# Performance work log

Hardware: AMD Instinct MI355X
Metric: run time of the kernel (lower is better)

The kernel has to match this reference:

```python
import jax, jax.numpy as jnp
import numpy as np


def _unfold(x, k):
    # x: [B, C, H, W] -> [B, C, S, L] with S=k*k (row-major patch order), L=H*W
    B, C, H, W = x.shape
    pad = k // 2
    xp = jnp.pad(x, ((0, 0), (0, 0), (pad, pad), (pad, pad)))
    patches = jnp.stack(
        [xp[:, :, r:r + H, c:c + W] for r in range(k) for c in range(k)], axis=2
    )  # [B, C, S, H, W]
    return patches.reshape(B, C, k * k, H * W)


def setup_inputs() -> dict:
    key = jax.random.key(0)
    ks = jax.random.split(key, 8)
    B, C, H, W = 8, 64, 128, 128
    R, Cout = 4, 128
    x = jax.random.normal(ks[0], (B, C, H, W), dtype=jnp.float32)
    gate_w = jax.random.normal(ks[1], (R, C), dtype=jnp.float32) * 0.05   # 1x1 gate conv weight
    gate_b = jax.random.normal(ks[2], (R,), dtype=jnp.float32) * 0.01
    theta = jax.random.normal(ks[3], (R,), dtype=jnp.float32) * 0.5       # learned directions
    raw_sigma_u = jax.random.normal(ks[4], (R,), dtype=jnp.float32) * 0.1
    raw_sigma_s = jax.random.normal(ks[5], (R,), dtype=jnp.float32) * 0.1
    pw_w = jax.random.normal(ks[6], (Cout, R * C), dtype=jnp.float32) * (1.0 / np.sqrt(R * C).astype(np.float32))
    pw_b = jax.random.normal(ks[7], (Cout,), dtype=jnp.float32) * 0.01
    return {"x": x, "gate_w": gate_w, "gate_b": gate_b, "theta": theta,
            "raw_sigma_u": raw_sigma_u, "raw_sigma_s": raw_sigma_s,
            "pw_w": pw_w, "pw_b": pw_b}


def reference(x, gate_w, gate_b, theta, raw_sigma_u, raw_sigma_s, pw_w, pw_b):
    k = 3
    B, C, H, W = x.shape
    R = theta.shape[0]
    S, L = k * k, H * W

    x_un = _unfold(x, k)                                         # [B, C, S, L]

    # 1x1 gate conv + fuzzy softmax over rules
    logits = jnp.einsum('bchw,rc->brhw', x, gate_w) + gate_b[None, :, None, None]
    mu = jax.nn.softmax(logits, axis=1)                          # [B, R, H, W]
    mu_un = _unfold(mu, k)                                       # [B, R, S, L]
    s_center = (k // 2) * k + (k // 2)
    mu_center = mu_un[:, :, s_center:s_center + 1, :]            # [B, R, 1, L]

    # anisotropic Gaussian kernel per rule over integer offsets (row-major)
    grid = np.arange(k, dtype=np.float32) - k // 2
    dy = jnp.asarray(np.repeat(grid, k))                         # [S]
    dx = jnp.asarray(np.tile(grid, k))                           # [S]
    cos_t, sin_t = jnp.cos(theta)[:, None], jnp.sin(theta)[:, None]
    proj_u = cos_t * dx[None, :] + sin_t * dy[None, :]           # [R, S]
    proj_s = -sin_t * dx[None, :] + cos_t * dy[None, :]
    su = (jax.nn.softplus(raw_sigma_u) + 1e-4)[:, None]
    ss = (jax.nn.softplus(raw_sigma_s) + 1e-4)[:, None]
    kern = jnp.exp(-proj_u ** 2 / su ** 2 - proj_s ** 2 / ss ** 2)  # [R, S]

    alpha = mu_center * mu_un * kern[None, :, :, None]           # [B, R, S, L]
    alpha_sum = jnp.maximum(alpha.sum(axis=(1, 2), keepdims=True), 1e-8)
    alpha = alpha / alpha_sum

    agg = jnp.einsum('brsl,bcsl->brcl', alpha, x_un)             # [B, R, C, L]
    agg_flat = agg.reshape(B, R * C, L)
    out = jnp.einsum('bnl,on->bol', agg_flat, pw_w) + pw_b[None, :, None]
    return out.reshape(B, -1, H, W)
```

## Files before the change

kernel.cpp:

```cpp
#include <hip/hip_runtime.h>
#include <math.h>

#define CC 64
#define RR 4
#define HH 128
#define WW 128
#define BB 8
#define COUT 128
#define XST 72
#define ALS 44

typedef __attribute__((ext_vector_type(8))) short short8;
typedef __attribute__((ext_vector_type(4))) float f32x4;
typedef __attribute__((ext_vector_type(2))) float f32x2;

__device__ __forceinline__ unsigned short f2bf(float f) {
  unsigned u = __float_as_uint(f);
  u += 0x7fffu + ((u >> 16) & 1u);
  return (unsigned short)(u >> 16);
}
__device__ __forceinline__ float bf2f(unsigned short h) {
  return __uint_as_float(((unsigned)h) << 16);
}
__device__ __forceinline__ float blo(unsigned u) { return __uint_as_float(u << 16); }
__device__ __forceinline__ float bhi(unsigned u) { return __uint_as_float(u & 0xffff0000u); }
__device__ __forceinline__ int swzx(int cb, int sp) { return cb ^ ((sp >> 3) & 7); }
__device__ __forceinline__ int swza(int cb, int row) { return cb ^ ((row >> 3) & 3); }

__global__ __launch_bounds__(256) void k_pre(const float* __restrict__ theta,
                                             const float* __restrict__ rsu,
                                             const float* __restrict__ rss,
                                             const float* __restrict__ pw,
                                             const float* __restrict__ gw,
                                             float* __restrict__ wkern,
                                             unsigned short* __restrict__ pwb,
                                             unsigned short* __restrict__ gwb) {
  int i = blockIdx.x * 256 + threadIdx.x;
  if (i < COUT * RR * CC) pwb[i] = f2bf(pw[i]);
  if (blockIdx.x == 0 && threadIdx.x < RR * 9) {
    int t = threadIdx.x;
    int r = t / 9, s = t % 9;
    float dy = (float)(s / 3 - 1), dx = (float)(s % 3 - 1);
    float ct = cosf(theta[r]), st = sinf(theta[r]);
    float su = log1pf(expf(rsu[r])) + 1e-4f;
    float sv = log1pf(expf(rss[r])) + 1e-4f;
    float pu = ct * dx + st * dy;
    float ps = -st * dx + ct * dy;
    wkern[t] = expf(-(pu * pu) / (su * su) - (ps * ps) / (sv * sv));
  }
  if (blockIdx.x == 1) {
    #pragma unroll
    for (int k = 0; k < 4; ++k) {
      int j = k * 256 + threadIdx.x;
      gwb[j] = (j < RR * CC) ? f2bf(gw[j]) : (unsigned short)0;
    }
  }
}

__global__ __launch_bounds__(256, 3) void k_fused(const float* __restrict__ x,
                                                  const float* __restrict__ gb,
                                                  const float* __restrict__ wkern,
                                                  const unsigned short* __restrict__ pwb,
                                                  const unsigned short* __restrict__ gwb,
                                                  const float* __restrict__ pb,
                                                  float* __restrict__ out) {
  __shared__ unsigned short xsT[160][XST];
  __shared__ unsigned short mus[RR][4][40];
  __shared__ unsigned short alp[64][ALS];
  __shared__ float rsum[RR][64];
  __shared__ __align__(16) unsigned short aggs[16][264];

  int tid = threadIdx.x;
  int raw = blockIdx.x;
  int bid = (raw & 7) * 256 + (raw >> 3);
  int b = bid >> 8;
  int rem = bid & 255;
  int h0 = (rem >> 2) << 1;
  int w0 = (rem & 3) << 5;

  int lane = tid & 63;
  int wv = tid >> 6;
  int lr = lane & 15, lq = lane >> 4;
  int o0 = wv << 5;

  short8 a0r[8], a1r[8];
  {
    const unsigned short* pA = pwb + ((o0 + lr) << 8) + (lq << 3);
    #pragma unroll
    for (int ks = 0; ks < 8; ++ks) {
      a0r[ks] = *(const short8*)(pA + (ks << 5));
      a1r[ks] = *(const short8*)(pA + 4096 + (ks << 5));
    }
  }
  short8 am0 = *(const short8*)(gwb + (lr << 6) + (lq << 3));
  short8 am1 = *(const short8*)(gwb + (lr << 6) + 32 + (lq << 3));
  float4 pbv0 = *(const float4*)&pb[o0 + (lq << 2)];
  float4 pbv1 = *(const float4*)&pb[o0 + 16 + (lq << 2)];
  float gb0 = gb[0], gb1 = gb[1], gb2 = gb[2], gb3 = gb[3];

  #pragma unroll
  for (int k = 0; k < 3; ++k) {
    int item = k * 256 + tid;
    if (item < 640) {
      int c4 = item % 10;
      int rest = item / 10;
      int row = rest & 3, cquad = rest >> 2;
      int c = cquad << 2;
      int gcol = w0 - 4 + (c4 << 2);
      int grow = h0 - 1 + row;
      float4 v0 = make_float4(0.f,0.f,0.f,0.f), v1 = v0, v2 = v0, v3 = v0;
      if ((unsigned)gcol < WW && (unsigned)grow < HH) {
        const float* xp = x + (((size_t)b * CC + c) << 14) + (grow << 7) + gcol;
        v0 = *(const float4*)xp;
        v1 = *(const float4*)(xp + (1 << 14));
        v2 = *(const float4*)(xp + (2 << 14));
        v3 = *(const float4*)(xp + (3 << 14));
      }
      int spb = row * 40 + (c4 << 2);
      int cb = cquad >> 1, sub = (cquad & 1) << 2;
      float4 vv[4] = {v0, v1, v2, v3};
      #pragma unroll
      for (int j = 0; j < 4; ++j) {
        int sp = spb + j;
        float f0 = (&vv[0].x)[j], f1 = (&vv[1].x)[j], f2v = (&vv[2].x)[j], f3 = (&vv[3].x)[j];
        ushort4 uv;
        uv.x = f2bf(f0); uv.y = f2bf(f1); uv.z = f2bf(f2v); uv.w = f2bf(f3);
        *(ushort4*)&xsT[sp][(swzx(cb, sp) << 3) + sub] = uv;
      }
    }
  }
  __syncthreads();

  for (int j = wv; j < 9; j += 4) {
    int p = (j << 4) + lr;
    int pcl = p > 135 ? 135 : p;
    unsigned y = (unsigned)pcl / 34u;
    int cxo = pcl - (int)(y * 34u);
    int pos = (int)y * 40 + 3 + cxo;
    short8 b0 = *(const short8*)&xsT[pos][swzx(lq, pos) << 3];
    short8 b1 = *(const short8*)&xsT[pos][swzx(4 + lq, pos) << 3];
    f32x4 mac = (f32x4){0.f, 0.f, 0.f, 0.f};
    mac = __builtin_amdgcn_mfma_f32_16x16x32_bf16(am0, b0, mac, 0, 0, 0);
    mac = __builtin_amdgcn_mfma_f32_16x16x32_bf16(am1, b1, mac, 0, 0, 0);
    if (lq == 0 && p < 136) {
      int grow = h0 - 1 + (int)y, gcol = w0 - 1 + cxo;
      float lg0 = mac[0] + gb0, lg1 = mac[1] + gb1;
      float lg2 = mac[2] + gb2, lg3 = mac[3] + gb3;
      float m = fmaxf(fmaxf(lg0, lg1), fmaxf(lg2, lg3));
      float e0 = expf(lg0 - m), e1 = expf(lg1 - m);
      float e2 = expf(lg2 - m), e3 = expf(lg3 - m);
      float inv = 1.0f / (e0 + e1 + e2 + e3);
      if (!((unsigned)grow < HH && (unsigned)gcol < WW)) inv = 0.0f;
      mus[0][y][3 + cxo] = f2bf(e0 * inv);
      mus[1][y][3 + cxo] = f2bf(e1 * inv);
      mus[2][y][3 + cxo] = f2bf(e2 * inv);
      mus[3][y][3 + cxo] = f2bf(e3 * inv);
    }
  }
  __syncthreads();

  {
    int t = tid & 63, r = tid >> 6;
    int prow = t >> 5, pcol = t & 31;
    float mc = bf2f(mus[r][prow + 1][pcol + 4]);
    float sum = 0.f;
    #pragma unroll
    for (int s = 0; s < 9; ++s) {
      float av = mc * bf2f(mus[r][prow + s / 3][pcol + 3 + s % 3]) * wkern[r * 9 + s];
      alp[t][(s << 2) + r] = f2bf(av);
      sum += av;
    }
    rsum[r][t] = sum;
  }
  __syncthreads();

  f32x4 dprev0 = (f32x4){0.f, 0.f, 0.f, 0.f};
  f32x4 dprev1 = (f32x4){0.f, 0.f, 0.f, 0.f};
  #pragma unroll
  for (int rd = 0; rd < 4; ++rd) {
    {
      int t16 = tid & 15, cg = tid >> 4;
      int px = (rd << 4) + t16;
      int prow2 = px >> 5, pc = px & 31;
      float inv = 1.0f / fmaxf(rsum[0][px] + rsum[1][px] + rsum[2][px] + rsum[3][px], 1e-8f);

      uint2 ad[9];
      #pragma unroll
      for (int s = 0; s < 9; ++s) ad[s] = *(const uint2*)(&alp[px][s << 2]);

      f32x2 cacc[4][2];
      #pragma unroll
      for (int r = 0; r < 4; ++r) {
        cacc[r][0] = (f32x2){0.f, 0.f};
        cacc[r][1] = (f32x2){0.f, 0.f};
      }

      int cb = cg >> 1, sub = (cg & 1) << 2;
      #pragma unroll
      for (int s = 0; s < 9; ++s) {
        int sp = (prow2 + s / 3) * 40 + pc + 3 + s % 3;
        uint2 ux = *(const uint2*)&xsT[sp][(swzx(cb, sp) << 3) + sub];
        f32x2 xv0 = {blo(ux.x), bhi(ux.x)};
        f32x2 xv1 = {blo(ux.y), bhi(ux.y)};
        unsigned adx = ad[s].x, ady = ad[s].y;
        float af0 = blo(adx), af1 = bhi(adx), af2 = blo(ady), af3 = bhi(ady);
        f32x2 A0 = {af0, af0}, A1 = {af1, af1}, A2 = {af2, af2}, A3 = {af3, af3};
        cacc[0][0] += A0 * xv0; cacc[0][1] += A0 * xv1;
        cacc[1][0] += A1 * xv0; cacc[1][1] += A1 * xv1;
        cacc[2][0] += A2 * xv0; cacc[2][1] += A2 * xv1;
        cacc[3][0] += A3 * xv0; cacc[3][1] += A3 * xv1;
      }
      #pragma unroll
      for (int r = 0; r < 4; ++r) {
        ushort4 wvv;
        wvv.x = f2bf(cacc[r][0][0] * inv); wvv.y = f2bf(cacc[r][0][1] * inv);
        wvv.z = f2bf(cacc[r][1][0] * inv); wvv.w = f2bf(cacc[r][1][1] * inv);
        int kb = (r << 3) + cb;
        *(ushort4*)&aggs[t16][(swza(kb, t16) << 3) + sub] = wvv;
      }
    }
    __syncthreads();

    {
      f32x4 dacc0 = (f32x4){0.f, 0.f, 0.f, 0.f};
      f32x4 dacc1 = (f32x4){0.f, 0.f, 0.f, 0.f};
      #pragma unroll
      for (int ks = 0; ks < 8; ++ks) {
        short8 b0 = *(const short8*)&aggs[lr][swza((ks << 2) + lq, lr) << 3];
        dacc0 = __builtin_amdgcn_mfma_f32_16x16x32_bf16(a0r[ks], b0, dacc0, 0, 0, 0);
        dacc1 = __builtin_amdgcn_mfma_f32_16x16x32_bf16(a1r[ks], b0, dacc1, 0, 0, 0);
      }
      if ((rd & 1) == 0) {
        dprev0 = dacc0; dprev1 = dacc1;
      } else {
        int orow = h0 + (rd >> 1);
        #pragma unroll
        for (int q = 0; q < 4; ++q) {
          int o = o0 + (lq << 2) + q;
          size_t base0 = (((size_t)b * COUT + o) << 14) + (orow << 7) + w0;
          size_t base1 = (((size_t)b * COUT + o + 16) << 14) + (orow << 7) + w0;
          out[base0 + lr]      = dprev0[q] + pbv0[q];
          out[base0 + 16 + lr] = dacc0[q] + pbv0[q];
          out[base1 + lr]      = dprev1[q] + pbv1[q];
          out[base1 + 16 + lr] = dacc1[q] + pbv1[q];
        }
      }
    }
    if (rd < 3) __syncthreads();
  }
}

extern "C" void kernel_launch(void* const* d_in, const int* in_sizes, int n_in,
                              void* d_out, int out_size, void* d_ws, size_t ws_size,
                              hipStream_t stream) {
  const float* x     = (const float*)d_in[0];
  const float* gw    = (const float*)d_in[1];
  const float* gb    = (const float*)d_in[2];
  const float* theta = (const float*)d_in[3];
  const float* rsu   = (const float*)d_in[4];
  const float* rss   = (const float*)d_in[5];
  const float* pw    = (const float*)d_in[6];
  const float* pb    = (const float*)d_in[7];
  float* outp = (float*)d_out;

  float* wkern = (float*)d_ws;
  unsigned short* pwb = (unsigned short*)(wkern + 64);
  unsigned short* gwb = pwb + COUT * RR * CC;

  k_pre<<<128, 256, 0, stream>>>(theta, rsu, rss, pw, gw, wkern, pwb, gwb);
  k_fused<<<BB * (HH / 2) * (WW / 32), 256, 0, stream>>>(x, gb, wkern, pwb, gwb, pb, outp);
}
```

Before: 54.38 us.

## Enlarge fused tile to 4x32 pixels with 512-thread blocks

Each block now covers a 4-row by 32-column output tile instead of 2x32, and runs 512 threads (8 waves) instead of 256. The 3x3 halo overhead per output pixel drops: 6 input rows are staged per 4 output rows instead of 4 per 2. Each wave now handles 16 output channels, holding half the pointwise-weight registers and issuing two MFMAs per k-step over two 16-pixel column groups. Each aggregation round covers a full 32-pixel row, so results are written directly without buffering the previous round. The cost is larger shared memory per block and fewer blocks in the grid, which may lower occupancy and load balance.

```diff
diff --git a/kernel.cpp b/kernel.cpp
--- a/kernel.cpp
+++ b/kernel.cpp
@@ -57,54 +57,51 @@
   }
 }
 
-__global__ __launch_bounds__(256, 3) void k_fused(const float* __restrict__ x,
+__global__ __launch_bounds__(512, 4) void k_fused(const float* __restrict__ x,
                                                   const float* __restrict__ gb,
                                                   const float* __restrict__ wkern,
                                                   const unsigned short* __restrict__ pwb,
                                                   const unsigned short* __restrict__ gwb,
                                                   const float* __restrict__ pb,
                                                   float* __restrict__ out) {
-  __shared__ unsigned short xsT[160][XST];
-  __shared__ unsigned short mus[RR][4][40];
-  __shared__ unsigned short alp[64][ALS];
-  __shared__ float rsum[RR][64];
-  __shared__ __align__(16) unsigned short aggs[16][264];
+  __shared__ unsigned short xsT[240][XST];
+  __shared__ unsigned short mus[RR][6][40];
+  __shared__ unsigned short alp[128][ALS];
+  __shared__ float rsum[RR][128];
+  __shared__ __align__(16) unsigned short aggs[32][264];
 
   int tid = threadIdx.x;
   int raw = blockIdx.x;
-  int bid = (raw & 7) * 256 + (raw >> 3);
-  int b = bid >> 8;
-  int rem = bid & 255;
-  int h0 = (rem >> 2) << 1;
+  int bid = (raw & 7) * 128 + (raw >> 3);
+  int b = bid >> 7;
+  int rem = bid & 127;
+  int h0 = (rem >> 2) << 2;
   int w0 = (rem & 3) << 5;
 
   int lane = tid & 63;
   int wv = tid >> 6;
   int lr = lane & 15, lq = lane >> 4;
-  int o0 = wv << 5;
-
-  short8 a0r[8], a1r[8];
+  int o0 = wv << 4;
+
+  short8 a0r[8];
   {
     const unsigned short* pA = pwb + ((o0 + lr) << 8) + (lq << 3);
     #pragma unroll
-    for (int ks = 0; ks < 8; ++ks) {
-      a0r[ks] = *(const short8*)(pA + (ks << 5));
-      a1r[ks] = *(const short8*)(pA + 4096 + (ks << 5));
-    }
+    for (int ks = 0; ks < 8; ++ks) a0r[ks] = *(const short8*)(pA + (ks << 5));
   }
   short8 am0 = *(const short8*)(gwb + (lr << 6) + (lq << 3));
   short8 am1 = *(const short8*)(gwb + (lr << 6) + 32 + (lq << 3));
-  float4 pbv0 = *(const float4*)&pb[o0 + (lq << 2)];
-  float4 pbv1 = *(const float4*)&pb[o0 + 16 + (lq << 2)];
+  float4 pbv = *(const float4*)&pb[o0 + (lq << 2)];
   float gb0 = gb[0], gb1 = gb[1], gb2 = gb[2], gb3 = gb[3];
 
   #pragma unroll
-  for (int k = 0; k < 3; ++k) {
-    int item = k * 256 + tid;
-    if (item < 640) {
+  for (int k = 0; k < 2; ++k) {
+    int item = k * 512 + tid;
+    if (item < 960) {
       int c4 = item % 10;
       int rest = item / 10;
-      int row = rest & 3, cquad = rest >> 2;
+      int cquad = rest / 6;
+      int row = rest - cquad * 6;
       int c = cquad << 2;
       int gcol = w0 - 4 + (c4 << 2);
       int grow = h0 - 1 + row;
@@ -131,9 +128,9 @@
   }
   __syncthreads();
 
-  for (int j = wv; j < 9; j += 4) {
+  for (int j = wv; j < 13; j += 8) {
     int p = (j << 4) + lr;
-    int pcl = p > 135 ? 135 : p;
+    int pcl = p > 203 ? 203 : p;
     unsigned y = (unsigned)pcl / 34u;
     int cxo = pcl - (int)(y * 34u);
     int pos = (int)y * 40 + 3 + cxo;
@@ -142,7 +139,7 @@
     f32x4 mac = (f32x4){0.f, 0.f, 0.f, 0.f};
     mac = __builtin_amdgcn_mfma_f32_16x16x32_bf16(am0, b0, mac, 0, 0, 0);
     mac = __builtin_amdgcn_mfma_f32_16x16x32_bf16(am1, b1, mac, 0, 0, 0);
-    if (lq == 0 && p < 136) {
+    if (lq == 0 && p < 204) {
       int grow = h0 - 1 + (int)y, gcol = w0 - 1 + cxo;
       float lg0 = mac[0] + gb0, lg1 = mac[1] + gb1;
       float lg2 = mac[2] + gb2, lg3 = mac[3] + gb3;
@@ -160,7 +157,7 @@
   __syncthreads();
 
   {
-    int t = tid & 63, r = tid >> 6;
+    int t = tid & 127, r = tid >> 7;
     int prow = t >> 5, pcol = t & 31;
     float mc = bf2f(mus[r][prow + 1][pcol + 4]);
     float sum = 0.f;
@@ -174,14 +171,10 @@
   }
   __syncthreads();
 
-  f32x4 dprev0 = (f32x4){0.f, 0.f, 0.f, 0.f};
-  f32x4 dprev1 = (f32x4){0.f, 0.f, 0.f, 0.f};
-  #pragma unroll
   for (int rd = 0; rd < 4; ++rd) {
     {
-      int t16 = tid & 15, cg = tid >> 4;
-      int px = (rd << 4) + t16;
-      int prow2 = px >> 5, pc = px & 31;
+      int t = tid & 31, cg = tid >> 5;
+      int px = (rd << 5) + t;
       float inv = 1.0f / fmaxf(rsum[0][px] + rsum[1][px] + rsum[2][px] + rsum[3][px], 1e-8f);
 
       uint2 ad[9];
@@ -198,7 +191,7 @@
       int cb = cg >> 1, sub = (cg & 1) << 2;
       #pragma unroll
       for (int s = 0; s < 9; ++s) {
-        int sp = (prow2 + s / 3) * 40 + pc + 3 + s % 3;
+        int sp = (rd + s / 3) * 40 + t + 3 + s % 3;
         uint2 ux = *(const uint2*)&xsT[sp][(swzx(cb, sp) << 3) + sub];
         f32x2 xv0 = {blo(ux.x), bhi(ux.x)};
         f32x2 xv1 = {blo(ux.y), bhi(ux.y)};
@@ -216,7 +209,7 @@
         wvv.x = f2bf(cacc[r][0][0] * inv); wvv.y = f2bf(cacc[r][0][1] * inv);
         wvv.z = f2bf(cacc[r][1][0] * inv); wvv.w = f2bf(cacc[r][1][1] * inv);
         int kb = (r << 3) + cb;
-        *(ushort4*)&aggs[t16][(swza(kb, t16) << 3) + sub] = wvv;
+        *(ushort4*)&aggs[t][(swza(kb, t) << 3) + sub] = wvv;
       }
     }
     __syncthreads();
@@ -227,23 +220,17 @@
       #pragma unroll
       for (int ks = 0; ks < 8; ++ks) {
         short8 b0 = *(const short8*)&aggs[lr][swza((ks << 2) + lq, lr) << 3];
+        short8 b1 = *(const short8*)&aggs[16 + lr][swza((ks << 2) + lq, 16 + lr) << 3];
         dacc0 = __builtin_amdgcn_mfma_f32_16x16x32_bf16(a0r[ks], b0, dacc0, 0, 0, 0);
-        dacc1 = __builtin_amdgcn_mfma_f32_16x16x32_bf16(a1r[ks], b0, dacc1, 0, 0, 0);
-      }
-      if ((rd & 1) == 0) {
-        dprev0 = dacc0; dprev1 = dacc1;
-      } else {
-        int orow = h0 + (rd >> 1);
-        #pragma unroll
-        for (int q = 0; q < 4; ++q) {
-          int o = o0 + (lq << 2) + q;
-          size_t base0 = (((size_t)b * COUT + o) << 14) + (orow << 7) + w0;
-          size_t base1 = (((size_t)b * COUT + o + 16) << 14) + (orow << 7) + w0;
-          out[base0 + lr]      = dprev0[q] + pbv0[q];
-          out[base0 + 16 + lr] = dacc0[q] + pbv0[q];
-          out[base1 + lr]      = dprev1[q] + pbv1[q];
-          out[base1 + 16 + lr] = dacc1[q] + pbv1[q];
-        }
+        dacc1 = __builtin_amdgcn_mfma_f32_16x16x32_bf16(a0r[ks], b1, dacc1, 0, 0, 0);
+      }
+      int orow = h0 + rd;
+      #pragma unroll
+      for (int q = 0; q < 4; ++q) {
+        int o = o0 + (lq << 2) + q;
+        size_t base = (((size_t)b * COUT + o) << 14) + (orow << 7) + w0;
+        out[base + lr]      = dacc0[q] + pbv[q];
+        out[base + 16 + lr] = dacc1[q] + pbv[q];
       }
     }
     if (rd < 3) __syncthreads();
@@ -268,5 +255,5 @@
   unsigned short* gwb = pwb + COUT * RR * CC;
 
   k_pre<<<128, 256, 0, stream>>>(theta, rsu, rss, pw, gw, wkern, pwb, gwb);
-  k_fused<<<BB * (HH / 2) * (WW / 32), 256, 0, stream>>>(x, gb, wkern, pwb, gwb, pb, outp);
-}
+  k_fused<<<BB * (HH / 4) * (WW / 32), 512, 0, stream>>>(x, gb, wkern, pwb, gwb, pb, outp);
+}
```

After: 50.57 us, median of 2. 1.08x faster.
